# Kernel optimization log

Hardware: AMD Instinct MI355X
Metric: run time of the kernel (lower is better)

The kernel has to match this reference:

```python
import jax, jax.numpy as jnp
import numpy as np

B, S, D, H = 4, 2048, 1024, 16
DK = D // H
SCALE = float(np.sqrt(DK))
NEG_INF = jnp.float32(-1e30)


def setup_inputs() -> dict:
    key = jax.random.key(0)
    ks = jax.random.split(key, 12)
    std = 1.0 / np.sqrt(D)
    def lin(k):
        kw, kb = jax.random.split(k)
        W = jax.random.uniform(kw, (D, D), jnp.float32, -std, std)
        b = jax.random.uniform(kb, (D,), jnp.float32, -std, std)
        return W, b
    Wq, bq = lin(ks[0]); Wk, bk = lin(ks[1]); Wv, bv = lin(ks[2]); Wo, bo = lin(ks[3])
    query = jax.random.normal(ks[4], (B, S, D), jnp.float32)
    key_t = jax.random.normal(ks[5], (B, S, D), jnp.float32)
    value = jax.random.normal(ks[6], (B, S, D), jnp.float32)
    # causal mask, broadcastable to [B,H,S,S]; positions where mask==0 are blocked
    mask = jnp.tril(jnp.ones((S, S), dtype=bool))[None, None]
    return {"query": query, "key": key_t, "value": value,
            "Wq": Wq, "bq": bq, "Wk": Wk, "bk": bk, "Wv": Wv, "bv": bv,
            "Wo": Wo, "bo": bo, "mask": mask}


def reference(query, key, value, Wq, bq, Wk, bk, Wv, bv, Wo, bo, mask):
    # projections: x @ W.T + b (torch nn.Linear convention)
    q = (query @ Wq.T + bq).reshape(B, S, H, DK).transpose(0, 2, 1, 3)  # [B,H,S,DK]
    k = (key @ Wk.T + bk).reshape(B, S, H, DK).transpose(0, 2, 1, 3)
    v = (value @ Wv.T + bv).reshape(B, S, H, DK).transpose(0, 2, 1, 3)
    scores = jnp.einsum('bhqd,bhkd->bhqk', q, k) / SCALE  # [B,H,S,S]
    scores = jnp.where(mask, scores, NEG_INF)
    attn = jax.nn.softmax(scores, axis=-1)
    # dropout is identity in eval / p used at train only; omitted (p treated as 0)
    context = jnp.einsum('bhqk,bhkd->bhqd', attn, v)  # [B,H,S,DK]
    context = context.transpose(0, 2, 1, 3).reshape(B, S, D)
    return context @ Wo.T + bo
```

## Files before the change

kernel.cpp:

```cpp
#include <hip/hip_runtime.h>
#include <hip/hip_bf16.h>
#include <cstdint>
#include <cstddef>


namespace {

constexpr int B  = 4;
constexpr int S  = 2048;
constexpr int D  = 1024;
constexpr int H  = 16;
constexpr int DK = 64;
constexpr int M  = B * S;
constexpr float LOG2E     = 1.44269504088896f;
constexpr float QSCALE    = 0.125f * LOG2E;
constexpr float NEG_BIG   = -1e30f;
constexpr float DEFER_THR = 8.0f;

using bf16 = __hip_bfloat16;

typedef __attribute__((ext_vector_type(8))) __bf16 bf16x8;
typedef __attribute__((ext_vector_type(4))) float  f32x4;

__device__ __forceinline__ uint16_t f2bfu(float x) {
  uint32_t a = __builtin_bit_cast(uint32_t, x);
  return (uint16_t)((a + 0x7FFFu + ((a >> 16) & 1u)) >> 16);
}
__device__ __forceinline__ uint32_t pk2(float x, float y) {
  return (uint32_t)f2bfu(x) | ((uint32_t)f2bfu(y) << 16);
}
__device__ __forceinline__ float ex2(float x) {
  float r; asm("v_exp_f32 %0, %1" : "=v"(r) : "v"(x)); return r;
}
__device__ __forceinline__ uint32_t cvtpk(float lo, float hi) {
  uint32_t r;
  asm("v_cvt_pk_bf16_f32 %0, %1, %2" : "=v"(r) : "v"(lo), "v"(hi));
  return r;
}
__device__ __forceinline__ float hmax4(f32x4 v) {
  return fmaxf(fmaxf(v[0], v[1]), fmaxf(v[2], v[3]));
}

__device__ __forceinline__ void ldst16(const uint4* g, uint4* l) {
  __builtin_amdgcn_global_load_lds(
      (const __attribute__((address_space(1))) void*)g,
      (__attribute__((address_space(3))) void*)l, 16, 0, 0);
}

__global__ __launch_bounds__(256)
void cvt3(const float* __restrict__ a, const float* __restrict__ b,
          const float* __restrict__ c, bf16* __restrict__ x,
          bf16* __restrict__ y, bf16* __restrict__ z_, int n8)
{
  const int zz = blockIdx.y;
  const float* src = (zz == 0) ? a : (zz == 1) ? b : c;
  bf16*        dst = (zz == 0) ? x : (zz == 1) ? y : z_;
  const int i = blockIdx.x * 256 + threadIdx.x;
  if (i >= n8) return;
  const float4 p = ((const float4*)src)[2 * i];
  const float4 q = ((const float4*)src)[2 * i + 1];
  uint4 r;
  r.x = pk2(p.x, p.y); r.y = pk2(p.z, p.w);
  r.z = pk2(q.x, q.y); r.w = pk2(q.z, q.w);
  ((uint4*)dst)[i] = r;
}

__global__ __launch_bounds__(256)
void cvt4(const float* __restrict__ a, const float* __restrict__ b,
          const float* __restrict__ c, const float* __restrict__ d,
          bf16* __restrict__ dst, int n8)
{
  const int zz = blockIdx.y;
  const float* src = (zz == 0) ? a : (zz == 1) ? b : (zz == 2) ? c : d;
  bf16* out = dst + (size_t)zz * n8 * 8;
  const int i = blockIdx.x * 256 + threadIdx.x;
  if (i >= n8) return;
  const float4 p = ((const float4*)src)[2 * i];
  const float4 q = ((const float4*)src)[2 * i + 1];
  uint4 r;
  r.x = pk2(p.x, p.y); r.y = pk2(p.z, p.w);
  r.z = pk2(q.x, q.y); r.w = pk2(q.z, q.w);
  ((uint4*)out)[i] = r;
}

__global__ __launch_bounds__(256, 3)
void proj_qkv(const bf16* __restrict__ Aq, const bf16* __restrict__ Ak,
              const bf16* __restrict__ Av, const bf16* __restrict__ Wall,
              const float* __restrict__ bq_, const float* __restrict__ bk_,
              const float* __restrict__ bv_, bf16* __restrict__ qo,
              bf16* __restrict__ ko, bf16* __restrict__ vto)
{
  __shared__ uint4 AsU[1024];
  __shared__ uint4 BsU[1024];

  const int z = blockIdx.z;
  const bf16*  A    = (z == 0) ? Aq : (z == 1) ? Ak : Av;
  const bf16*  Wb   = Wall + (size_t)z * D * D;
  const float* bias = (z == 0) ? bq_ : (z == 1) ? bk_ : bv_;

  const int tid  = threadIdx.x;
  const int w    = tid >> 6;
  const int lane = tid & 63;
  const int lm   = lane & 15;
  const int quad = lane >> 4;
  const int wm   = (w >> 1) * 64;
  const int wn   = (w & 1) * 64;

  const int row0 = blockIdx.y * 128, col0 = blockIdx.x * 128;
  constexpr int g8 = D >> 3;

  const uint4* Ag = (const uint4*)A + (size_t)row0 * g8;
  const uint4* Bg = (const uint4*)Wb + (size_t)col0 * g8;

  f32x4 acc[4][4] = {};

  for (int kt = 0; kt < D / 64; ++kt) {
    __syncthreads();
#pragma unroll
    for (int i = 0; i < 4; ++i) {
      const int chunk = i * 256 + w * 64 + lane;
      const int r = chunk >> 3, c = chunk & 7;
      ldst16(&Ag[(size_t)r * g8 + kt * 8 + c], &AsU[i * 256 + w * 64]);
      ldst16(&Bg[(size_t)r * g8 + kt * 8 + c], &BsU[i * 256 + w * 64]);
    }
    __syncthreads();
#pragma unroll
    for (int kk = 0; kk < 2; ++kk) {
      bf16x8 af[4], bfr[4];
#pragma unroll
      for (int tm = 0; tm < 4; ++tm)
        af[tm] = __builtin_bit_cast(bf16x8, AsU[(wm + tm * 16 + lm) * 8 + kk * 4 + quad]);
#pragma unroll
      for (int tn = 0; tn < 4; ++tn)
        bfr[tn] = __builtin_bit_cast(bf16x8, BsU[(wn + tn * 16 + lm) * 8 + kk * 4 + quad]);
#pragma unroll
      for (int tm = 0; tm < 4; ++tm)
#pragma unroll
        for (int tn = 0; tn < 4; ++tn)
          acc[tm][tn] = __builtin_amdgcn_mfma_f32_16x16x32_bf16(af[tm], bfr[tn], acc[tm][tn], 0, 0, 0);
    }
  }

  const float scale = (z == 0) ? QSCALE : 1.0f;
#pragma unroll
  for (int tm = 0; tm < 4; ++tm) {
#pragma unroll
    for (int tn = 0; tn < 4; ++tn) {
      const int col = col0 + wn + tn * 16 + lm;
      const float bv = bias[col];
      if (z == 2) {
        float vv[4];
#pragma unroll
        for (int r = 0; r < 4; ++r) vv[r] = acc[tm][tn][r] + bv;
        const int s0 = row0 + wm + tm * 16 + quad * 4;
        const int b_ = s0 >> 11, ss = s0 & (S - 1);
        const int h_ = col >> 6, dk = col & (DK - 1);
        uint2 st; st.x = pk2(vv[0], vv[1]); st.y = pk2(vv[2], vv[3]);
        *(uint2*)(vto + (((size_t)b_ * H + h_) * DK + dk) * S + ss) = st;
      } else {
        bf16* out = (z == 0) ? qo : ko;
#pragma unroll
        for (int r = 0; r < 4; ++r) {
          const int row = row0 + wm + tm * 16 + quad * 4 + r;
          const float v = (acc[tm][tn][r] + bv) * scale;
          const int b_ = row >> 11, s_ = row & (S - 1);
          const int h_ = col >> 6,  dk = col & (DK - 1);
          out[(((size_t)b_ * H + h_) * S + s_) * DK + dk] =
              __builtin_bit_cast(bf16, f2bfu(v));
        }
      }
    }
  }
}

template <int MODE>
__global__ __launch_bounds__(256)
void gemm128(const bf16* __restrict__ A, const bf16* __restrict__ Wb,
             const float* __restrict__ bias, void* __restrict__ out,
             int N, int K, float scale)
{
  __shared__ uint4 AsU[2][1024];
  __shared__ uint4 BsU[2][1024];

  const int tid  = threadIdx.x;
  const int w    = tid >> 6;
  const int lane = tid & 63;
  const int lm   = lane & 15;
  const int quad = lane >> 4;
  const int wm   = (w >> 1) * 64;
  const int wn   = (w & 1) * 64;

  const int row0 = blockIdx.y * 128, col0 = blockIdx.x * 128;
  const int g8 = K >> 3;

  const uint4* Ag = (const uint4*)A + (size_t)row0 * g8;
  const uint4* Bg = (const uint4*)Wb + (size_t)col0 * g8;

  f32x4 acc[4][4] = {};
  const int KT = K / 64;

#pragma unroll
  for (int i = 0; i < 4; ++i) {
    const int chunk = i * 256 + w * 64 + lane;
    const int r = chunk >> 3, c = chunk & 7;
    ldst16(&Ag[(size_t)r * g8 + c], &AsU[0][i * 256 + w * 64]);
    ldst16(&Bg[(size_t)r * g8 + c], &BsU[0][i * 256 + w * 64]);
  }

  int cur = 0;
  for (int kt = 0; kt < KT; ++kt) {
    __syncthreads();
    if (kt + 1 < KT) {
#pragma unroll
      for (int i = 0; i < 4; ++i) {
        const int chunk = i * 256 + w * 64 + lane;
        const int r = chunk >> 3, c = chunk & 7;
        ldst16(&Ag[(size_t)r * g8 + (kt + 1) * 8 + c], &AsU[cur ^ 1][i * 256 + w * 64]);
        ldst16(&Bg[(size_t)r * g8 + (kt + 1) * 8 + c], &BsU[cur ^ 1][i * 256 + w * 64]);
      }
    }
#pragma unroll
    for (int kk = 0; kk < 2; ++kk) {
      bf16x8 af[4], bfr[4];
#pragma unroll
      for (int tm = 0; tm < 4; ++tm)
        af[tm] = __builtin_bit_cast(bf16x8, AsU[cur][(wm + tm * 16 + lm) * 8 + kk * 4 + quad]);
#pragma unroll
      for (int tn = 0; tn < 4; ++tn)
        bfr[tn] = __builtin_bit_cast(bf16x8, BsU[cur][(wn + tn * 16 + lm) * 8 + kk * 4 + quad]);
#pragma unroll
      for (int tm = 0; tm < 4; ++tm)
#pragma unroll
        for (int tn = 0; tn < 4; ++tn)
          acc[tm][tn] = __builtin_amdgcn_mfma_f32_16x16x32_bf16(af[tm], bfr[tn], acc[tm][tn], 0, 0, 0);
    }
    cur ^= 1;
  }

#pragma unroll
  for (int tm = 0; tm < 4; ++tm) {
#pragma unroll
    for (int tn = 0; tn < 4; ++tn) {
      const int col = col0 + wn + tn * 16 + lm;
      const float bv = bias[col];
      if (MODE == 2) {
        float vv[4];
#pragma unroll
        for (int r = 0; r < 4; ++r) vv[r] = (acc[tm][tn][r] + bv) * scale;
        const int s0 = row0 + wm + tm * 16 + quad * 4;
        const int b_ = s0 >> 11, ss = s0 & (S - 1);
        const int h_ = col >> 6, dk = col & (DK - 1);
        uint2 st; st.x = pk2(vv[0], vv[1]); st.y = pk2(vv[2], vv[3]);
        *(uint2*)((bf16*)out + (((size_t)b_ * H + h_) * DK + dk) * S + ss) = st;
      } else {
#pragma unroll
        for (int r = 0; r < 4; ++r) {
          const int row = row0 + wm + tm * 16 + quad * 4 + r;
          const float v = (acc[tm][tn][r] + bv) * scale;
          if (MODE == 0) {
            ((float*)out)[(size_t)row * N + col] = v;
          } else {
            const int b_ = row >> 11, s_ = row & (S - 1);
            const int h_ = col >> 6,  dk = col & (DK - 1);
            ((bf16*)out)[(((size_t)b_ * H + h_) * S + s_) * DK + dk] =
                __builtin_bit_cast(bf16, f2bfu(v));
          }
        }
      }
    }
  }
}

__global__ __launch_bounds__(512)
void flash_mfma(const bf16* __restrict__ Q, const bf16* __restrict__ K,
                const bf16* __restrict__ Vt, bf16* __restrict__ ctx)
{
  __shared__ uint4 KsU[2][512];
  __shared__ uint4 VtU[2][512];
  __shared__ uint16_t Os[128 * 72];

  const int tid  = threadIdx.x;
  const int w    = tid >> 6;
  const int lane = tid & 63;
  const int lm   = lane & 15;
  const int quad = lane >> 4;
  const int bh   = blockIdx.x;
  const int pr   = blockIdx.y;
  const size_t base = (size_t)bh * S * DK;

  const uint4* Kg0 = (const uint4*)(K + base);
  const uint4* Vg0 = (const uint4*)(Vt + (size_t)bh * DK * S);

  const int rr  = w * 8 + (lane >> 3);
  const int csw = (lane & 7) ^ (lane >> 3) ^ ((w & 1) << 2);
  const int fv  = (lm & 7) ^ (((lm >> 3) & 1) << 2);
  const int r0  = ((lm >> 2) << 3) | (lm & 3);

  uint16_t* const Ow = Os + (w * 16) * 72;
  const int b_ = bh >> 4, h_ = bh & (H - 1);

  for (int pass = 0; pass < 2; ++pass) {
    const int qi = pass ? (15 - pr) : pr;
    const int q0 = qi * 128;
    const int qbase = q0 + w * 16;

    bf16x8 qf0, qf1;
    {
      const bf16* qrow = Q + base + (size_t)(qbase + lm) * DK;
      qf0 = __builtin_bit_cast(bf16x8, *(const uint4*)(qrow + quad * 8));
      qf1 = __builtin_bit_cast(bf16x8, *(const uint4*)(qrow + 32 + quad * 8));
    }

    f32x4 o[4] = {};
    float m_i = NEG_BIG, l_i = 0.f;

    const int nt = 2 * qi + 2;

    ldst16(&Kg0[(size_t)rr * 8 + csw],       &KsU[0][w * 64]);
    ldst16(&Vg0[(size_t)rr * (S / 8) + csw], &VtU[0][w * 64]);

    int cur = 0;
    for (int t = 0; t < nt; ++t) {
      __syncthreads();
      if (t + 1 < nt) {
        const int k1 = (t + 1) * 64;
        ldst16(&Kg0[(size_t)(k1 + rr) * 8 + csw],         &KsU[cur ^ 1][w * 64]);
        ldst16(&Vg0[(size_t)rr * (S / 8) + k1 / 8 + csw], &VtU[cur ^ 1][w * 64]);
      }
      const int k0 = t * 64;
      if (k0 <= qbase + 15) {
        const uint4* Ks = KsU[cur];
        const uint4* Vs = VtU[cur];

        f32x4 sc[4];
        __builtin_amdgcn_s_setprio(1);
#pragma unroll
        for (int tn = 0; tn < 4; ++tn) {
          const int row = r0 + ((tn & 1) << 2) + ((tn >> 1) << 5);
          const int fr  = (row & 7) ^ (((row >> 3) & 1) << 2);
          const int cb  = quad ^ fr;
          bf16x8 kb0 = __builtin_bit_cast(bf16x8, Ks[row * 8 + cb]);
          bf16x8 kb1 = __builtin_bit_cast(bf16x8, Ks[row * 8 + (cb ^ 4)]);
          sc[tn] = __builtin_amdgcn_mfma_f32_16x16x32_bf16(
                       kb0, qf0, f32x4{0.f, 0.f, 0.f, 0.f}, 0, 0, 0);
          sc[tn] = __builtin_amdgcn_mfma_f32_16x16x32_bf16(kb1, qf1, sc[tn], 0, 0, 0);
        }
        __builtin_amdgcn_s_setprio(0);

        if (k0 + 63 > qbase) {
          const int qg = qbase + lm;
#pragma unroll
          for (int tn = 0; tn < 4; ++tn) {
            const int kb_ = k0 + ((tn >> 1) << 5) + (quad << 3) + ((tn & 1) << 2);
#pragma unroll
            for (int r = 0; r < 4; ++r)
              if (kb_ + r > qg) sc[tn][r] = NEG_BIG;
          }
        }

        float mloc = fmaxf(fmaxf(hmax4(sc[0]), hmax4(sc[1])),
                           fmaxf(hmax4(sc[2]), hmax4(sc[3])));
        mloc = fmaxf(mloc, __shfl_xor(mloc, 16));
        mloc = fmaxf(mloc, __shfl_xor(mloc, 32));

        if (__any(mloc > m_i + DEFER_THR)) {
          const float mn = fmaxf(m_i, mloc);
          const float al = ex2(m_i - mn);
          l_i *= al; m_i = mn;
          const float a0 = __shfl(al, quad * 4 + 0, 16);
          const float a1 = __shfl(al, quad * 4 + 1, 16);
          const float a2 = __shfl(al, quad * 4 + 2, 16);
          const float a3 = __shfl(al, quad * 4 + 3, 16);
#pragma unroll
          for (int tn = 0; tn < 4; ++tn) {
            o[tn][0] *= a0; o[tn][1] *= a1; o[tn][2] *= a2; o[tn][3] *= a3;
          }
        }

        float ls = 0.f;
#pragma unroll
        for (int tn = 0; tn < 4; ++tn) {
#pragma unroll
          for (int r = 0; r < 4; ++r) sc[tn][r] = ex2(sc[tn][r] - m_i);
          ls += (sc[tn][0] + sc[tn][1]) + (sc[tn][2] + sc[tn][3]);
        }
        l_i += ls;

        uint4 pw0, pw1;
        pw0.x = cvtpk(sc[0][0], sc[0][1]); pw0.y = cvtpk(sc[0][2], sc[0][3]);
        pw0.z = cvtpk(sc[1][0], sc[1][1]); pw0.w = cvtpk(sc[1][2], sc[1][3]);
        pw1.x = cvtpk(sc[2][0], sc[2][1]); pw1.y = cvtpk(sc[2][2], sc[2][3]);
        pw1.z = cvtpk(sc[3][0], sc[3][1]); pw1.w = cvtpk(sc[3][2], sc[3][3]);
        const bf16x8 ap0 = __builtin_bit_cast(bf16x8, pw0);
        const bf16x8 ap1 = __builtin_bit_cast(bf16x8, pw1);

        __builtin_amdgcn_s_setprio(1);
#pragma unroll
        for (int tn = 0; tn < 4; ++tn) {
          const int vrow = tn * 16 + lm;
          const int cv = quad ^ fv;
          bf16x8 vb0 = __builtin_bit_cast(bf16x8, Vs[vrow * 8 + cv]);
          bf16x8 vb1 = __builtin_bit_cast(bf16x8, Vs[vrow * 8 + (cv ^ 4)]);
          o[tn] = __builtin_amdgcn_mfma_f32_16x16x32_bf16(ap0, vb0, o[tn], 0, 0, 0);
          o[tn] = __builtin_amdgcn_mfma_f32_16x16x32_bf16(ap1, vb1, o[tn], 0, 0, 0);
        }
        __builtin_amdgcn_s_setprio(0);
      }
      cur ^= 1;
    }

    __syncthreads();
    {
      float lr = l_i;
      lr += __shfl_xor(lr, 16);
      lr += __shfl_xor(lr, 32);
      const float inv = 1.f / lr;
      const float i0 = __shfl(inv, quad * 4 + 0, 16);
      const float i1 = __shfl(inv, quad * 4 + 1, 16);
      const float i2 = __shfl(inv, quad * 4 + 2, 16);
      const float i3 = __shfl(inv, quad * 4 + 3, 16);
#pragma unroll
      for (int tn = 0; tn < 4; ++tn) {
        Ow[(quad * 4 + 0) * 72 + tn * 16 + lm] = f2bfu(o[tn][0] * i0);
        Ow[(quad * 4 + 1) * 72 + tn * 16 + lm] = f2bfu(o[tn][1] * i1);
        Ow[(quad * 4 + 2) * 72 + tn * 16 + lm] = f2bfu(o[tn][2] * i2);
        Ow[(quad * 4 + 3) * 72 + tn * 16 + lm] = f2bfu(o[tn][3] * i3);
      }
    }
    __syncthreads();

#pragma unroll
    for (int i = 0; i < 2; ++i) {
      const int idx = tid + i * 512;
      const int row = idx >> 3, c = idx & 7;
      const uint4 v = *(const uint4*)(Os + row * 72 + c * 8);
      *(uint4*)(ctx + ((((size_t)b_ * S + q0 + row) * H + h_) << 6) + c * 8) = v;
    }
  }
}

}

extern "C" void kernel_launch(void* const* d_in, const int* in_sizes, int n_in,
                              void* d_out, int out_size, void* d_ws, size_t ws_size,
                              hipStream_t stream)
{
  const float* query = (const float*)d_in[0];
  const float* key_  = (const float*)d_in[1];
  const float* value = (const float*)d_in[2];
  const float* Wq    = (const float*)d_in[3];
  const float* bq    = (const float*)d_in[4];
  const float* Wk    = (const float*)d_in[5];
  const float* bk    = (const float*)d_in[6];
  const float* Wv    = (const float*)d_in[7];
  const float* bv    = (const float*)d_in[8];
  const float* Wo    = (const float*)d_in[9];
  const float* bo    = (const float*)d_in[10];

  const size_t qkv = (size_t)B * H * S * DK;
  const size_t DD  = (size_t)D * D;
  bf16* slot0 = (bf16*)d_ws;
  bf16* slot1 = slot0 + qkv;
  bf16* slot2 = slot1 + qkv;
  bf16* slot3 = slot2 + qkv;
  bf16* slot4 = slot3 + qkv;
  bf16* dout0 = (bf16*)d_out;
  bf16* dout1 = dout0 + qkv;

  const int n8in = (int)(qkv / 8);
  const int n8w  = (int)(DD / 8);
  const dim3 gproj(D / 128, M / 128);
  const dim3 gattn(B * H, 8);

  const size_t need = (4 * qkv + 4 * DD) * sizeof(bf16);

  if (ws_size >= need) {
    cvt3<<<dim3(n8in / 256, 3), 256, 0, stream>>>(query, key_, value,
                                                  dout0, dout1, slot3, n8in);
    cvt4<<<dim3(n8w / 256, 4), 256, 0, stream>>>(Wq, Wk, Wv, Wo, slot4, n8w);
    proj_qkv<<<dim3(D / 128, M / 128, 3), 256, 0, stream>>>(
        dout0, dout1, slot3, slot4, bq, bk, bv, slot0, slot1, slot2);
    flash_mfma<<<gattn, 512, 0, stream>>>(slot0, slot1, slot2, slot3);
    gemm128<0><<<gproj, 256, 0, stream>>>(slot3, slot4 + 3 * DD, bo, d_out,
                                          D, D, 1.0f);
  } else {
    cvt3<<<dim3(n8in / 256, 3), 256, 0, stream>>>(query, key_, value,
                                                  dout0, dout1, slot3, n8in);
    cvt3<<<dim3(n8w / 256, 2), 256, 0, stream>>>(Wq, Wk, Wk,
                                                 slot2, slot2 + DD, slot2, n8w);
    gemm128<1><<<gproj, 256, 0, stream>>>(dout0, slot2, bq, slot0, D, D, QSCALE);
    gemm128<1><<<gproj, 256, 0, stream>>>(dout1, slot2 + DD, bk, slot1, D, D, 1.0f);
    cvt3<<<dim3(n8w / 256, 1), 256, 0, stream>>>(Wv, Wv, Wv,
                                                 dout0, dout0, dout0, n8w);
    gemm128<2><<<gproj, 256, 0, stream>>>(slot3, dout0, bv, slot2, D, D, 1.0f);
    flash_mfma<<<gattn, 512, 0, stream>>>(slot0, slot1, slot2, slot3);
    cvt3<<<dim3(n8w / 256, 1), 256, 0, stream>>>(Wo, Wo, Wo,
                                                 slot0, slot0, slot0, n8w);
    gemm128<0><<<gproj, 256, 0, stream>>>(slot3, slot0, bo, d_out, D, D, 1.0f);
  }
}
```

Baseline: 325.8 us.

## Fuse fp32-to-bf16 input conversion into QKV projection and remap blocks for XCD locality

The QKV projection now reads the fp32 activations directly, converts them to bf16 in registers and writes them to LDS, with the next k-tile held in registers as a prefetch. This removes the separate cvt3 conversion kernel and its round trip of bf16 copies through global memory. It also adds an XCD-aware remap of block indices in the projection and output GEMMs so that neighbouring tiles share L2. The costs are more register pressure from the eight float4 prefetch registers, synchronous global loads for A in place of the async global_load_lds path, and an LDS write pattern that may cause bank conflicts.

```diff
diff --git a/kernel.cpp b/kernel.cpp
--- a/kernel.cpp
+++ b/kernel.cpp
@@ -45,6 +45,12 @@
   __builtin_amdgcn_global_load_lds(
       (const __attribute__((address_space(1))) void*)g,
       (__attribute__((address_space(3))) void*)l, 16, 0, 0);
+}
+
+__device__ __forceinline__ void xcd_remap(int& bx, int& by) {
+  const int orig = blockIdx.x + (blockIdx.y << 3);
+  bx = (orig >> 3) & 7;
+  by = ((orig & 7) << 3) + (orig >> 6);
 }
 
 __global__ __launch_bounds__(256)
@@ -84,8 +90,8 @@
 }
 
 __global__ __launch_bounds__(256, 3)
-void proj_qkv(const bf16* __restrict__ Aq, const bf16* __restrict__ Ak,
-              const bf16* __restrict__ Av, const bf16* __restrict__ Wall,
+void proj_qkv(const float* __restrict__ Aq, const float* __restrict__ Ak,
+              const float* __restrict__ Av, const bf16* __restrict__ Wall,
               const float* __restrict__ bq_, const float* __restrict__ bk_,
               const float* __restrict__ bv_, bf16* __restrict__ qo,
               bf16* __restrict__ ko, bf16* __restrict__ vto)
@@ -94,7 +100,7 @@
   __shared__ uint4 BsU[1024];
 
   const int z = blockIdx.z;
-  const bf16*  A    = (z == 0) ? Aq : (z == 1) ? Ak : Av;
+  const float* A    = (z == 0) ? Aq : (z == 1) ? Ak : Av;
   const bf16*  Wb   = Wall + (size_t)z * D * D;
   const float* bias = (z == 0) ? bq_ : (z == 1) ? bk_ : bv_;
 
@@ -106,22 +112,42 @@
   const int wm   = (w >> 1) * 64;
   const int wn   = (w & 1) * 64;
 
-  const int row0 = blockIdx.y * 128, col0 = blockIdx.x * 128;
+  int bx, by; xcd_remap(bx, by);
+  const int row0 = by * 128, col0 = bx * 128;
   constexpr int g8 = D >> 3;
-
-  const uint4* Ag = (const uint4*)A + (size_t)row0 * g8;
+  constexpr int KT = D / 64;
+
   const uint4* Bg = (const uint4*)Wb + (size_t)col0 * g8;
 
+  const int t16r = tid >> 4, t16c = tid & 15;
+  const float* Ap = A + (size_t)(row0 + t16r) * D + t16c * 4;
+  uint32_t* const As32 = (uint32_t*)AsU;
+
   f32x4 acc[4][4] = {};
-
-  for (int kt = 0; kt < D / 64; ++kt) {
+  float4 av[8];
+
+#pragma unroll
+  for (int p = 0; p < 8; ++p)
+    av[p] = *(const float4*)(Ap + (size_t)p * 16 * D);
+
+  for (int kt = 0; kt < KT; ++kt) {
     __syncthreads();
 #pragma unroll
     for (int i = 0; i < 4; ++i) {
       const int chunk = i * 256 + w * 64 + lane;
       const int r = chunk >> 3, c = chunk & 7;
-      ldst16(&Ag[(size_t)r * g8 + kt * 8 + c], &AsU[i * 256 + w * 64]);
       ldst16(&Bg[(size_t)r * g8 + kt * 8 + c], &BsU[i * 256 + w * 64]);
+    }
+#pragma unroll
+    for (int p = 0; p < 8; ++p) {
+      const int idx = ((t16r + 16 * p) << 4) + t16c;
+      ((uint2*)As32)[idx] = uint2{cvtpk(av[p].x, av[p].y),
+                                  cvtpk(av[p].z, av[p].w)};
+    }
+    if (kt + 1 < KT) {
+#pragma unroll
+      for (int p = 0; p < 8; ++p)
+        av[p] = *(const float4*)(Ap + (size_t)p * 16 * D + (kt + 1) * 64);
     }
     __syncthreads();
 #pragma unroll
@@ -190,7 +216,8 @@
   const int wm   = (w >> 1) * 64;
   const int wn   = (w & 1) * 64;
 
-  const int row0 = blockIdx.y * 128, col0 = blockIdx.x * 128;
+  int bx, by; xcd_remap(bx, by);
+  const int row0 = by * 128, col0 = bx * 128;
   const int g8 = K >> 3;
 
   const uint4* Ag = (const uint4*)A + (size_t)row0 * g8;
@@ -475,11 +502,9 @@
   const size_t need = (4 * qkv + 4 * DD) * sizeof(bf16);
 
   if (ws_size >= need) {
-    cvt3<<<dim3(n8in / 256, 3), 256, 0, stream>>>(query, key_, value,
-                                                  dout0, dout1, slot3, n8in);
     cvt4<<<dim3(n8w / 256, 4), 256, 0, stream>>>(Wq, Wk, Wv, Wo, slot4, n8w);
     proj_qkv<<<dim3(D / 128, M / 128, 3), 256, 0, stream>>>(
-        dout0, dout1, slot3, slot4, bq, bk, bv, slot0, slot1, slot2);
+        query, key_, value, slot4, bq, bk, bv, slot0, slot1, slot2);
     flash_mfma<<<gattn, 512, 0, stream>>>(slot0, slot1, slot2, slot3);
     gemm128<0><<<gproj, 256, 0, stream>>>(slot3, slot4 + 3 * DD, bo, d_out,
                                           D, D, 1.0f);
```

New measurement: 334.6 us. +2.7%, slower.
